# Kernel tuning notes

Measured on AMD Instinct MI355X. Metric: run time of the kernel, lower is better.

## Reference

```python
import jax, jax.numpy as jnp
import numpy as np
from jax import lax

N = 100000
IN_C, HID, OUT_C = 512, 256, 128
K_STEPS = 10
ALPHA = 0.1
RES_ALPHA = 1.0
LN_EPS = 1e-5


def layer_norm(h, g, b):
    mu = jnp.mean(h, axis=-1, keepdims=True)
    var = jnp.mean(jnp.square(h - mu), axis=-1, keepdims=True)
    return (h - mu) * lax.rsqrt(var + LN_EPS) * g + b


def appnp(h, src, dst):
    # add self loops
    loop = jnp.arange(N, dtype=src.dtype)
    s = jnp.concatenate([src, loop])
    d = jnp.concatenate([dst, loop])
    ew = jnp.ones(s.shape[0], h.dtype)
    deg = jax.ops.segment_sum(ew, d, num_segments=N)
    dis = jnp.where(deg > 0, lax.rsqrt(jnp.maximum(deg, 1e-12)), 0.0)
    norm = dis[s] * ew * dis[d]  # [E+N]
    h0 = h
    def step(carry, _):
        msg = norm[:, None] * carry[s]                      # gather [E+N, C]
        agg = jax.ops.segment_sum(msg, d, num_segments=N)    # scatter-add
        return (1.0 - ALPHA) * agg + ALPHA * h0, None
    h, _ = lax.scan(step, h, None, length=K_STEPS)
    return h


def setup_inputs() -> dict:
    key = jax.random.key(0)
    ks = jax.random.split(key, 12)
    def lin(k, fan_in, fan_out):
        bound = 1.0 / np.sqrt(fan_in)
        kw, kb = jax.random.split(k)
        W = jax.random.uniform(kw, (fan_in, fan_out), jnp.float32, -bound, bound)
        b = jax.random.uniform(kb, (fan_out,), jnp.float32, -bound, bound)
        return W, b
    x = jax.random.normal(ks[0], (N, IN_C), jnp.float32)
    edge_index = jax.random.randint(ks[1], (2, 1600000), 0, N, jnp.int32)
    W_in, b_in = lin(ks[2], IN_C, HID)
    W1, b1 = lin(ks[3], HID, HID)
    W2, b2 = lin(ks[4], HID, HID)
    W_out, b_out = lin(ks[5], HID, OUT_C)
    g1 = jnp.ones(HID); be1 = jnp.zeros(HID)
    g2 = jnp.ones(HID); be2 = jnp.zeros(HID)
    return {"x": x, "edge_index": edge_index,
            "W_in": W_in, "b_in": b_in,
            "W1": W1, "b1": b1, "g1": g1, "be1": be1,
            "W2": W2, "b2": b2, "g2": g2, "be2": be2,
            "W_out": W_out, "b_out": b_out}


def reference(x, edge_index, W_in, b_in, W1, b1, g1, be1, W2, b2, g2, be2, W_out, b_out):
    # MLP with residual blocks (eval mode: no dropout)
    h = x @ W_in + b_in
    for (W, b, g, be) in ((W1, b1, g1, be1), (W2, b2, g2, be2)):
        identity = h
        h = layer_norm(h @ W + b, g, be)
        h = RES_ALPHA * h + (1.0 - RES_ALPHA) * identity
        h = jax.nn.relu(h)
    h = h @ W_out + b_out
    # APPNP propagation
    return appnp(h, edge_index[0], edge_index[1])
```

## Files before the change

### kernel.cpp

```cpp
#include <hip/hip_runtime.h>

typedef unsigned short u16;
typedef __attribute__((ext_vector_type(8))) short bfrag;
typedef __attribute__((ext_vector_type(4))) float f32x4;

__device__ inline float b2f(u16 u) {
    union { unsigned int i; float f; } v; v.i = ((unsigned int)u) << 16; return v.f;
}
__device__ inline u16 f2b(float f) {
    union { float f; unsigned int u; } v; v.f = f;
    unsigned int r = v.u + 0x7fffu + ((v.u >> 16) & 1u);
    return (u16)(r >> 16);
}
__device__ inline float ldF(const void* p, size_t i, bool bf) {
    return bf ? b2f(((const u16*)p)[i]) : ((const float*)p)[i];
}
__device__ inline void gload_lds16(const void* g, void* l) {
    __builtin_amdgcn_global_load_lds((const __attribute__((address_space(1))) unsigned int*)g,
                                     (__attribute__((address_space(3))) unsigned int*)l, 16, 0, 0);
}

__global__ void detect_k(const unsigned int* __restrict__ g1w, int* flag) {
    if (blockIdx.x == 0 && threadIdx.x == 0)
        *flag = (g1w[0] == 0x3F803F80u) ? 1 : 0;
}

__global__ void cvt_x(const void* __restrict__ in, u16* __restrict__ out, int n4,
                      const int* __restrict__ flagp) {
    int i = blockIdx.x * 256 + threadIdx.x;
    if (i >= n4) return;
    if (*flagp) {
        ((ushort4*)out)[i] = ((const ushort4*)in)[i];
    } else {
        const float4 v = ((const float4*)in)[i];
        ushort4 o; o.x = f2b(v.x); o.y = f2b(v.y); o.z = f2b(v.z); o.w = f2b(v.w);
        ((ushort4*)out)[i] = o;
    }
}

__global__ void wt_k(const void* __restrict__ W, u16* __restrict__ Wt, int K, int NC,
                     const int* __restrict__ flagp) {
    int i = blockIdx.x * 256 + threadIdx.x;
    if (i >= K * NC) return;
    int k = i / NC, nn = i - k * NC;
    u16 v = (*flagp) ? ((const u16*)W)[i] : f2b(((const float*)W)[i]);
    Wt[(size_t)nn * K + k] = v;
}

template<int K, bool OUT_BF16>
__global__ __launch_bounds__(256) void gemm_bt(const u16* __restrict__ A, const u16* __restrict__ Bt,
                                               const void* __restrict__ bias, void* __restrict__ C,
                                               int M, int NC, const int* __restrict__ flagp) {
    const int BM = 128, BN = 128, BK = 32;
    __shared__ u16 As[2][BM * BK];
    __shared__ u16 Bs[2][BN * BK];
    const bool bf = (*flagp != 0);
    int nt = NC / BN;

    int nwg = gridDim.x, bid = blockIdx.x;
    int qc = nwg >> 3, rc = nwg & 7;
    int xcd = bid & 7, off = bid >> 3;
    int swz = (xcd < rc ? xcd * (qc + 1) : rc * (qc + 1) + (xcd - rc) * qc) + off;
    int m0 = (swz / nt) * BM;
    int n0 = (swz % nt) * BN;

    int t = threadIdx.x;
    int lane = t & 63, wave = t >> 6;
    int wm = (wave >> 1) * 64, wn = (wave & 1) * 64;

    f32x4 acc[4][4];
#pragma unroll
    for (int i = 0; i < 4; i++)
#pragma unroll
        for (int j = 0; j < 4; j++) acc[i][j] = (f32x4){0.f, 0.f, 0.f, 0.f};

    auto stage = [&](int bufi, int kk) {
#pragma unroll
        for (int q = 0; q < 2; ++q) {
            int idx = q * 256 + t;
            int row = idx >> 2;
            int cb  = (idx & 3) * 16;
            int ra = m0 + row; ra = ra < M ? ra : M - 1;
            const char* ga = (const char*)A  + ((size_t)ra * K) * 2 + kk * 2 + cb;
            const char* gb = (const char*)Bt + ((size_t)(n0 + row) * K) * 2 + kk * 2 + cb;
            char* la = (char*)&As[bufi][0] + q * 4096 + wave * 1024;
            char* lb = (char*)&Bs[bufi][0] + q * 4096 + wave * 1024;
            gload_lds16(ga, la);
            gload_lds16(gb, lb);
        }
    };

    stage(0, 0);
    __syncthreads();
    int cur = 0;
    int r16 = lane & 15, q8 = (lane >> 4) * 8;
    for (int k0 = 0; k0 < K; k0 += BK) {
        if (k0 + BK < K) stage(cur ^ 1, k0 + BK);
        bfrag a[4], b[4];
#pragma unroll
        for (int i = 0; i < 4; i++) a[i] = *(const bfrag*)&As[cur][(wm + i * 16 + r16) * BK + q8];
#pragma unroll
        for (int j = 0; j < 4; j++) b[j] = *(const bfrag*)&Bs[cur][(wn + j * 16 + r16) * BK + q8];
#pragma unroll
        for (int i = 0; i < 4; i++)
#pragma unroll
            for (int j = 0; j < 4; j++)
                acc[i][j] = __builtin_amdgcn_mfma_f32_16x16x32_bf16(a[i], b[j], acc[i][j], 0, 0, 0);
        __syncthreads();
        cur ^= 1;
    }

    int q4 = (lane >> 4) * 4;
#pragma unroll
    for (int j = 0; j < 4; j++) {
        int cg = n0 + wn + j * 16 + r16;
        float bvv = ldF(bias, cg, bf);
#pragma unroll
        for (int i = 0; i < 4; i++) {
#pragma unroll
            for (int rr = 0; rr < 4; rr++) {
                int rg = m0 + wm + i * 16 + q4 + rr;
                if (rg < M) {
                    float v = acc[i][j][rr] + bvv;
                    if (OUT_BF16) ((u16*)C)[(size_t)rg * NC + cg] = f2b(v);
                    else          ((float*)C)[(size_t)rg * NC + cg] = v;
                }
            }
        }
    }
}

__global__ __launch_bounds__(256) void ln_relu_k(const float* __restrict__ T, const void* __restrict__ g,
                                                 const void* __restrict__ be, u16* __restrict__ out,
                                                 int M, const int* __restrict__ flagp) {
    const bool bf = (*flagp != 0);
    int wave = threadIdx.x >> 6, lane = threadIdx.x & 63;
    int row = blockIdx.x * 4 + wave;
    if (row >= M) return;
    const float4 x = *(const float4*)(T + (size_t)row * 256 + lane * 4);
    float s = x.x + x.y + x.z + x.w;
    for (int o = 32; o > 0; o >>= 1) s += __shfl_xor(s, o);
    float mu = s * (1.0f / 256.0f);
    float d0 = x.x - mu, d1 = x.y - mu, d2 = x.z - mu, d3 = x.w - mu;
    float q = d0 * d0 + d1 * d1 + d2 * d2 + d3 * d3;
    for (int o = 32; o > 0; o >>= 1) q += __shfl_xor(q, o);
    float rs = rsqrtf(q * (1.0f / 256.0f) + 1e-5f);
    int c0 = lane * 4;
    float y0 = fmaxf(d0 * rs * ldF(g, c0 + 0, bf) + ldF(be, c0 + 0, bf), 0.f);
    float y1 = fmaxf(d1 * rs * ldF(g, c0 + 1, bf) + ldF(be, c0 + 1, bf), 0.f);
    float y2 = fmaxf(d2 * rs * ldF(g, c0 + 2, bf) + ldF(be, c0 + 2, bf), 0.f);
    float y3 = fmaxf(d3 * rs * ldF(g, c0 + 3, bf) + ldF(be, c0 + 3, bf), 0.f);
    ushort4 o4; o4.x = f2b(y0); o4.y = f2b(y1); o4.z = f2b(y2); o4.w = f2b(y3);
    *(ushort4*)(out + (size_t)row * 256 + c0) = o4;
}

__global__ void deg_count(const int* __restrict__ dst, int* deg, int E) {
    int i = blockIdx.x * 256 + threadIdx.x;
    if (i < E) atomicAdd(&deg[dst[i]], 1);
}
__global__ void dis_k(const int* __restrict__ deg, float* dis, int n) {
    int i = blockIdx.x * 256 + threadIdx.x;
    if (i < n) dis[i] = rsqrtf((float)(deg[i] + 1));
}

__global__ void scan_block(const int* __restrict__ deg, int* rowptr, int* bsum, int n) {
    __shared__ int sh[256];
    int t = threadIdx.x, i = blockIdx.x * 256 + t;
    int v = (i < n) ? deg[i] + 1 : 0;
    sh[t] = v; __syncthreads();
    for (int o = 1; o < 256; o <<= 1) {
        int x = (t >= o) ? sh[t - o] : 0;
        __syncthreads();
        sh[t] += x;
        __syncthreads();
    }
    if (i < n) rowptr[i] = sh[t] - v;
    if (t == 255) bsum[blockIdx.x] = sh[t];
}
__global__ void scan_sums(int* bsum, int nb) {
    __shared__ int sh[512];
    int t = threadIdx.x;
    int v = (t < nb) ? bsum[t] : 0;
    sh[t] = v; __syncthreads();
    for (int o = 1; o < 512; o <<= 1) {
        int x = (t >= o) ? sh[t - o] : 0;
        __syncthreads();
        sh[t] += x;
        __syncthreads();
    }
    if (t < nb) bsum[t] = sh[t] - v;
}
__global__ void scan_add(int* rowptr, const int* __restrict__ bsum, int n, int total) {
    int i = blockIdx.x * 256 + threadIdx.x;
    if (i < n) rowptr[i] += bsum[blockIdx.x];
    if (i == 0) rowptr[n] = total;
}
__global__ void fill_k(const int* __restrict__ src, const int* __restrict__ dst,
                       const int* __restrict__ rowptr, int* cursor, const float* __restrict__ dis,
                       int2* __restrict__ epack, int E, int n) {
    int i = blockIdx.x * 256 + threadIdx.x;
    if (i >= E + n) return;
    int s, d;
    if (i < E) { s = src[i]; d = dst[i]; }
    else       { s = d = i - E; }
    int p = rowptr[d] + atomicAdd(&cursor[d], 1);
    float wv = dis[s] * dis[d];
    int2 e; e.x = s; e.y = __float_as_int(wv);
    epack[p] = e;
}

__global__ __launch_bounds__(256) void prop_k(const u16* __restrict__ curb, const u16* __restrict__ h0b,
                                              const int* __restrict__ rowptr, const int2* __restrict__ epack,
                                              u16* __restrict__ outB, void* __restrict__ outD,
                                              const int* __restrict__ flagp, int n) {
    int wave = threadIdx.x >> 6, lane = threadIdx.x & 63;
    int node = blockIdx.x * 4 + wave;
    if (node >= n) return;
    int p0 = rowptr[node], p1 = rowptr[node + 1];
    float ax = 0.f, ay = 0.f;
    for (int p = p0; p < p1; p += 64) {
        int cnt = p1 - p; if (cnt > 64) cnt = 64;
        int sj = 0; float wj = 0.f;
        if (lane < cnt) {
            int2 e = epack[p + lane];
            sj = e.x; wj = __int_as_float(e.y);
        }
        for (int j = 0; j < cnt; j += 16) {
            float ww[16]; unsigned int v[16];
#pragma unroll
            for (int u = 0; u < 16; ++u) {
                int jj = j + u;
                bool ok = jj < cnt;
                if (!ok) jj = cnt - 1;
                int ss = __shfl(sj, jj);
                float w = __shfl(wj, jj);
                ww[u] = ok ? w : 0.f;
                v[u] = *(const unsigned int*)(curb + (size_t)ss * 128 + 2 * lane);
            }
#pragma unroll
            for (int u = 0; u < 16; ++u) {
                ax = fmaf(ww[u], b2f((u16)(v[u] & 0xffffu)), ax);
                ay = fmaf(ww[u], b2f((u16)(v[u] >> 16)), ay);
            }
        }
    }
    unsigned int hp = ((const unsigned int*)h0b)[(size_t)node * 64 + lane];
    float rx = 0.9f * ax + 0.1f * b2f((u16)(hp & 0xffffu));
    float ry = 0.9f * ay + 0.1f * b2f((u16)(hp >> 16));
    if (outB) {
        unsigned int pk = ((unsigned int)f2b(ry) << 16) | (unsigned int)f2b(rx);
        ((unsigned int*)outB)[(size_t)node * 64 + lane] = pk;
    } else if (*flagp) {
        unsigned int pk = ((unsigned int)f2b(ry) << 16) | (unsigned int)f2b(rx);
        ((unsigned int*)outD)[(size_t)node * 64 + lane] = pk;
    } else {
        float2 o; o.x = rx; o.y = ry;
        *(float2*)((float*)outD + (size_t)node * 128 + 2 * lane) = o;
    }
}

extern "C" void kernel_launch(void* const* d_in, const int* in_sizes, int n_in,
                              void* d_out, int out_size, void* d_ws, size_t ws_size,
                              hipStream_t stream) {
    const int N = in_sizes[0] / 512;
    const int E = in_sizes[1] / 2;
    const void* x    = d_in[0];
    const int*  ei   = (const int*)d_in[1];
    const void* Win  = d_in[2];
    const void* bin  = d_in[3];
    const void* W1   = d_in[4];
    const void* b1   = d_in[5];
    const void* g1   = d_in[6];
    const void* be1  = d_in[7];
    const void* W2   = d_in[8];
    const void* b2   = d_in[9];
    const void* g2   = d_in[10];
    const void* be2  = d_in[11];
    const void* Wout = d_in[12];
    const void* bout = d_in[13];
    (void)n_in; (void)out_size; (void)ws_size;

    char* w = (char*)d_ws;
    auto alloc = [&](size_t b) { char* p = w; w += (b + 255) & ~(size_t)255; return p; };
    char*  buf0 = alloc((size_t)N * 512 * 2);
    char*  actAraw = alloc((size_t)N * 256 * 2);
    u16* WtIn  = (u16*)alloc((size_t)512 * 256 * 2);
    u16* Wt1   = (u16*)alloc((size_t)256 * 256 * 2);
    u16* Wt2   = (u16*)alloc((size_t)256 * 256 * 2);
    u16* WtOut = (u16*)alloc((size_t)256 * 128 * 2);
    int*   deg    = (int*)alloc((size_t)N * 4);
    float* dis    = (float*)alloc((size_t)N * 4);
    int*   rowptr = (int*)alloc((size_t)(N + 1) * 4);
    int*   cursor = (int*)alloc((size_t)N * 4);
    int*   bsum   = (int*)alloc(512 * 4);
    int*   flag   = (int*)alloc(256);
    u16*   xbf = (u16*)buf0;
    float* T   = (float*)buf0;
    u16*   h0b = (u16*)buf0;
    u16*   cA  = (u16*)(buf0 + (size_t)N * 128 * 2);
    u16*   cB  = (u16*)(buf0 + (size_t)N * 128 * 4);
    u16*   actA  = (u16*)actAraw;
    int2*  epack = (int2*)actAraw;

    detect_k<<<1, 64, 0, stream>>>((const unsigned int*)g1, flag);

    int n4 = N * 512 / 4;
    cvt_x<<<(n4 + 255) / 256, 256, 0, stream>>>(x, xbf, n4, flag);
    wt_k<<<(512 * 256 + 255) / 256, 256, 0, stream>>>(Win,  WtIn,  512, 256, flag);
    wt_k<<<(256 * 256 + 255) / 256, 256, 0, stream>>>(W1,   Wt1,   256, 256, flag);
    wt_k<<<(256 * 256 + 255) / 256, 256, 0, stream>>>(W2,   Wt2,   256, 256, flag);
    wt_k<<<(256 * 128 + 255) / 256, 256, 0, stream>>>(Wout, WtOut, 256, 128, flag);

    int mt = (N + 127) / 128;
    gemm_bt<512, true ><<<mt * 2, 256, 0, stream>>>(xbf,  WtIn,  bin,  actA, N, 256, flag);
    gemm_bt<256, false><<<mt * 2, 256, 0, stream>>>(actA, Wt1,   b1,   T,    N, 256, flag);
    ln_relu_k<<<(N + 3) / 4, 256, 0, stream>>>(T, g1, be1, actA, N, flag);
    gemm_bt<256, false><<<mt * 2, 256, 0, stream>>>(actA, Wt2,   b2,   T,    N, 256, flag);
    ln_relu_k<<<(N + 3) / 4, 256, 0, stream>>>(T, g2, be2, actA, N, flag);
    gemm_bt<256, true ><<<mt * 1, 256, 0, stream>>>(actA, WtOut, bout, h0b,  N, 128, flag);

    hipMemsetAsync(deg, 0, (size_t)N * 4, stream);
    deg_count<<<(E + 255) / 256, 256, 0, stream>>>(ei + E, deg, E);
    dis_k    <<<(N + 255) / 256, 256, 0, stream>>>(deg, dis, N);
    int nb = (N + 255) / 256;
    scan_block<<<nb, 256, 0, stream>>>(deg, rowptr, bsum, N);
    scan_sums<<<1, 512, 0, stream>>>(bsum, nb);
    scan_add<<<nb, 256, 0, stream>>>(rowptr, bsum, N, E + N);
    hipMemsetAsync(cursor, 0, (size_t)N * 4, stream);
    fill_k<<<(E + N + 255) / 256, 256, 0, stream>>>(ei, ei + E, rowptr, cursor, dis, epack, E, N);

    const u16* cur = h0b;
    for (int it = 0; it < 10; ++it) {
        bool last = (it == 9);
        u16* o = (it & 1) ? cB : cA;
        prop_k<<<(N + 3) / 4, 256, 0, stream>>>(cur, h0b, rowptr, epack,
                                                last ? nullptr : o,
                                                last ? d_out : nullptr, flag, N);
        cur = o;
    }
}
```

Baseline: 1.463 ms.

## Fuse x conversion into GEMM, bf16 LN intermediates, nontemporal prop loads

Drops the separate fp32-to-bf16 pass over x. When inputs are fp32, the first GEMM now loads floats and converts them to bf16 in its staging step. The GEMM outputs that feed LayerNorm are stored in bf16 rather than fp32, which halves that intermediate traffic at some cost in precision. The propagation kernel gets a full 16-wide unrolled gather loop plus a narrower tail loop, and uses nontemporal loads and stores for the edge list, h0 and outputs. In the fp32 path the first GEMM loses its async global-to-LDS load for A.

Measured after the change: 1.451 ms. Within noise of the previous version (-0.8%).

```diff
diff --git a/kernel.cpp b/kernel.cpp
--- a/kernel.cpp
+++ b/kernel.cpp
@@ -1,6 +1,7 @@
 #include <hip/hip_runtime.h>
 
 typedef unsigned short u16;
+typedef unsigned long long u64;
 typedef __attribute__((ext_vector_type(8))) short bfrag;
 typedef __attribute__((ext_vector_type(4))) float f32x4;
 
@@ -25,19 +26,6 @@
         *flag = (g1w[0] == 0x3F803F80u) ? 1 : 0;
 }
 
-__global__ void cvt_x(const void* __restrict__ in, u16* __restrict__ out, int n4,
-                      const int* __restrict__ flagp) {
-    int i = blockIdx.x * 256 + threadIdx.x;
-    if (i >= n4) return;
-    if (*flagp) {
-        ((ushort4*)out)[i] = ((const ushort4*)in)[i];
-    } else {
-        const float4 v = ((const float4*)in)[i];
-        ushort4 o; o.x = f2b(v.x); o.y = f2b(v.y); o.z = f2b(v.z); o.w = f2b(v.w);
-        ((ushort4*)out)[i] = o;
-    }
-}
-
 __global__ void wt_k(const void* __restrict__ W, u16* __restrict__ Wt, int K, int NC,
                      const int* __restrict__ flagp) {
     int i = blockIdx.x * 256 + threadIdx.x;
@@ -47,8 +35,8 @@
     Wt[(size_t)nn * K + k] = v;
 }
 
-template<int K, bool OUT_BF16>
-__global__ __launch_bounds__(256) void gemm_bt(const u16* __restrict__ A, const u16* __restrict__ Bt,
+template<int K, bool OUT_BF16, bool A_DUAL>
+__global__ __launch_bounds__(256) void gemm_bt(const void* __restrict__ Ain, const u16* __restrict__ Bt,
                                                const void* __restrict__ bias, void* __restrict__ C,
                                                int M, int NC, const int* __restrict__ flagp) {
     const int BM = 128, BN = 128, BK = 32;
@@ -81,11 +69,22 @@
             int row = idx >> 2;
             int cb  = (idx & 3) * 16;
             int ra = m0 + row; ra = ra < M ? ra : M - 1;
-            const char* ga = (const char*)A  + ((size_t)ra * K) * 2 + kk * 2 + cb;
             const char* gb = (const char*)Bt + ((size_t)(n0 + row) * K) * 2 + kk * 2 + cb;
             char* la = (char*)&As[bufi][0] + q * 4096 + wave * 1024;
             char* lb = (char*)&Bs[bufi][0] + q * 4096 + wave * 1024;
-            gload_lds16(ga, la);
+            if (!A_DUAL || bf) {
+                const char* ga = (const char*)Ain + ((size_t)ra * K) * 2 + kk * 2 + cb;
+                gload_lds16(ga, la);
+            } else {
+                const float* gaf = (const float*)Ain + (size_t)ra * K + kk + (cb >> 1);
+                float4 f0 = *(const float4*)gaf;
+                float4 f1 = *(const float4*)(gaf + 4);
+                ushort4 o0, o1;
+                o0.x = f2b(f0.x); o0.y = f2b(f0.y); o0.z = f2b(f0.z); o0.w = f2b(f0.w);
+                o1.x = f2b(f1.x); o1.y = f2b(f1.y); o1.z = f2b(f1.z); o1.w = f2b(f1.w);
+                *(ushort4*)(la + (size_t)lane * 16)     = o0;
+                *(ushort4*)(la + (size_t)lane * 16 + 8) = o1;
+            }
             gload_lds16(gb, lb);
         }
     };
@@ -130,18 +129,19 @@
     }
 }
 
-__global__ __launch_bounds__(256) void ln_relu_k(const float* __restrict__ T, const void* __restrict__ g,
+__global__ __launch_bounds__(256) void ln_relu_k(const u16* __restrict__ T, const void* __restrict__ g,
                                                  const void* __restrict__ be, u16* __restrict__ out,
                                                  int M, const int* __restrict__ flagp) {
     const bool bf = (*flagp != 0);
     int wave = threadIdx.x >> 6, lane = threadIdx.x & 63;
     int row = blockIdx.x * 4 + wave;
     if (row >= M) return;
-    const float4 x = *(const float4*)(T + (size_t)row * 256 + lane * 4);
-    float s = x.x + x.y + x.z + x.w;
+    const ushort4 xq = *(const ushort4*)(T + (size_t)row * 256 + lane * 4);
+    float x0 = b2f(xq.x), x1 = b2f(xq.y), x2 = b2f(xq.z), x3 = b2f(xq.w);
+    float s = x0 + x1 + x2 + x3;
     for (int o = 32; o > 0; o >>= 1) s += __shfl_xor(s, o);
     float mu = s * (1.0f / 256.0f);
-    float d0 = x.x - mu, d1 = x.y - mu, d2 = x.z - mu, d3 = x.w - mu;
+    float d0 = x0 - mu, d1 = x1 - mu, d2 = x2 - mu, d3 = x3 - mu;
     float q = d0 * d0 + d1 * d1 + d2 * d2 + d3 * d3;
     for (int o = 32; o > 0; o >>= 1) q += __shfl_xor(q, o);
     float rs = rsqrtf(q * (1.0f / 256.0f) + 1e-5f);
@@ -205,8 +205,8 @@
     else       { s = d = i - E; }
     int p = rowptr[d] + atomicAdd(&cursor[d], 1);
     float wv = dis[s] * dis[d];
-    int2 e; e.x = s; e.y = __float_as_int(wv);
-    epack[p] = e;
+    u64 e = ((u64)__float_as_uint(wv) << 32) | (unsigned int)s;
+    __builtin_nontemporal_store(e, (u64*)&epack[p]);
 }
 
 __global__ __launch_bounds__(256) void prop_k(const u16* __restrict__ curb, const u16* __restrict__ h0b,
@@ -222,40 +222,55 @@
         int cnt = p1 - p; if (cnt > 64) cnt = 64;
         int sj = 0; float wj = 0.f;
         if (lane < cnt) {
-            int2 e = epack[p + lane];
-            sj = e.x; wj = __int_as_float(e.y);
-        }
-        for (int j = 0; j < cnt; j += 16) {
+            u64 e = __builtin_nontemporal_load((const u64*)(epack + p + lane));
+            sj = (int)(unsigned int)e;
+            wj = __uint_as_float((unsigned int)(e >> 32));
+        }
+        int j = 0;
+        for (; j + 16 <= cnt; j += 16) {
             float ww[16]; unsigned int v[16];
 #pragma unroll
             for (int u = 0; u < 16; ++u) {
+                int ss = __shfl(sj, j + u);
+                ww[u] = __shfl(wj, j + u);
+                v[u] = *(const unsigned int*)(curb + (size_t)ss * 128 + 2 * lane);
+            }
+#pragma unroll
+            for (int u = 0; u < 16; ++u) {
+                ax = fmaf(ww[u], b2f((u16)(v[u] & 0xffffu)), ax);
+                ay = fmaf(ww[u], b2f((u16)(v[u] >> 16)), ay);
+            }
+        }
+        for (; j < cnt; j += 8) {
+            float ww[8]; unsigned int v[8];
+#pragma unroll
+            for (int u = 0; u < 8; ++u) {
                 int jj = j + u;
                 bool ok = jj < cnt;
                 if (!ok) jj = cnt - 1;
                 int ss = __shfl(sj, jj);
-                float w = __shfl(wj, jj);
-                ww[u] = ok ? w : 0.f;
+                float w2 = __shfl(wj, jj);
+                ww[u] = ok ? w2 : 0.f;
                 v[u] = *(const unsigned int*)(curb + (size_t)ss * 128 + 2 * lane);
             }
 #pragma unroll
-            for (int u = 0; u < 16; ++u) {
+            for (int u = 0; u < 8; ++u) {
                 ax = fmaf(ww[u], b2f((u16)(v[u] & 0xffffu)), ax);
                 ay = fmaf(ww[u], b2f((u16)(v[u] >> 16)), ay);
             }
         }
     }
-    unsigned int hp = ((const unsigned int*)h0b)[(size_t)node * 64 + lane];
+    unsigned int hp = __builtin_nontemporal_load((const unsigned int*)h0b + (size_t)node * 64 + lane);
     float rx = 0.9f * ax + 0.1f * b2f((u16)(hp & 0xffffu));
     float ry = 0.9f * ay + 0.1f * b2f((u16)(hp >> 16));
+    unsigned int pk = ((unsigned int)f2b(ry) << 16) | (unsigned int)f2b(rx);
     if (outB) {
-        unsigned int pk = ((unsigned int)f2b(ry) << 16) | (unsigned int)f2b(rx);
-        ((unsigned int*)outB)[(size_t)node * 64 + lane] = pk;
+        __builtin_nontemporal_store(pk, (unsigned int*)outB + (size_t)node * 64 + lane);
     } else if (*flagp) {
-        unsigned int pk = ((unsigned int)f2b(ry) << 16) | (unsigned int)f2b(rx);
-        ((unsigned int*)outD)[(size_t)node * 64 + lane] = pk;
+        __builtin_nontemporal_store(pk, (unsigned int*)outD + (size_t)node * 64 + lane);
     } else {
-        float2 o; o.x = rx; o.y = ry;
-        *(float2*)((float*)outD + (size_t)node * 128 + 2 * lane) = o;
+        u64 o = ((u64)__float_as_uint(ry) << 32) | __float_as_uint(rx);
+        __builtin_nontemporal_store(o, (u64*)((float*)outD + (size_t)node * 128 + 2 * lane));
     }
 }
 
@@ -294,8 +309,7 @@
     int*   cursor = (int*)alloc((size_t)N * 4);
     int*   bsum   = (int*)alloc(512 * 4);
     int*   flag   = (int*)alloc(256);
-    u16*   xbf = (u16*)buf0;
-    float* T   = (float*)buf0;
+    u16*   Tb  = (u16*)buf0;
     u16*   h0b = (u16*)buf0;
     u16*   cA  = (u16*)(buf0 + (size_t)N * 128 * 2);
     u16*   cB  = (u16*)(buf0 + (size_t)N * 128 * 4);
@@ -304,20 +318,18 @@
 
     detect_k<<<1, 64, 0, stream>>>((const unsigned int*)g1, flag);
 
-    int n4 = N * 512 / 4;
-    cvt_x<<<(n4 + 255) / 256, 256, 0, stream>>>(x, xbf, n4, flag);
     wt_k<<<(512 * 256 + 255) / 256, 256, 0, stream>>>(Win,  WtIn,  512, 256, flag);
     wt_k<<<(256 * 256 + 255) / 256, 256, 0, stream>>>(W1,   Wt1,   256, 256, flag);
     wt_k<<<(256 * 256 + 255) / 256, 256, 0, stream>>>(W2,   Wt2,   256, 256, flag);
     wt_k<<<(256 * 128 + 255) / 256, 256, 0, stream>>>(Wout, WtOut, 256, 128, flag);
 
     int mt = (N + 127) / 128;
-    gemm_bt<512, true ><<<mt * 2, 256, 0, stream>>>(xbf,  WtIn,  bin,  actA, N, 256, flag);
-    gemm_bt<256, false><<<mt * 2, 256, 0, stream>>>(actA, Wt1,   b1,   T,    N, 256, flag);
-    ln_relu_k<<<(N + 3) / 4, 256, 0, stream>>>(T, g1, be1, actA, N, flag);
-    gemm_bt<256, false><<<mt * 2, 256, 0, stream>>>(actA, Wt2,   b2,   T,    N, 256, flag);
-    ln_relu_k<<<(N + 3) / 4, 256, 0, stream>>>(T, g2, be2, actA, N, flag);
-    gemm_bt<256, true ><<<mt * 1, 256, 0, stream>>>(actA, WtOut, bout, h0b,  N, 128, flag);
+    gemm_bt<512, true , true ><<<mt * 2, 256, 0, stream>>>(x,    WtIn,  bin,  actA, N, 256, flag);
+    gemm_bt<256, true , false><<<mt * 2, 256, 0, stream>>>(actA, Wt1,   b1,   Tb,   N, 256, flag);
+    ln_relu_k<<<(N + 3) / 4, 256, 0, stream>>>(Tb, g1, be1, actA, N, flag);
+    gemm_bt<256, true , false><<<mt * 2, 256, 0, stream>>>(actA, Wt2,   b2,   Tb,   N, 256, flag);
+    ln_relu_k<<<(N + 3) / 4, 256, 0, stream>>>(Tb, g2, be2, actA, N, flag);
+    gemm_bt<256, true , false><<<mt * 1, 256, 0, stream>>>(actA, WtOut, bout, h0b,  N, 128, flag);
 
     hipMemsetAsync(deg, 0, (size_t)N * 4, stream);
     deg_count<<<(E + 255) / 256, 256, 0, stream>>>(ei + E, deg, E);
```
